# Kernel optimization log

Measured on AMD Instinct MI355X. Metric: run time of the kernel, lower is better.

The kernel has to match this reference:

```python
import jax, jax.numpy as jnp
import numpy as np

HEAD_DIM = 128
N_HEADS = 32
ROPE_DIM = 64
TOPK = 1024
B, S, HID, QLORA = 1, 2048, 4096, 1536
LN_EPS = 1e-5  # torch nn.LayerNorm default


def _hadamard_matrix(n):
    H = np.array([[1.0]], dtype=np.float32)
    while H.shape[0] < n:
        H = np.block([[H, H], [H, -H]])
    return jnp.asarray(H)

_H128 = _hadamard_matrix(HEAD_DIM)
_FWHT_SCALE = HEAD_DIM ** -0.5


def rotate_activation(x):
    # Fast Walsh-Hadamard transform == x @ H_sylvester, scaled by dim**-0.5
    return (x @ _H128) * _FWHT_SCALE


def rope_non_interleaved(x, cos, sin):
    # x: [..., rope_dim]; cos/sin: broadcastable [..., rope_dim/2]
    half = x.shape[-1] // 2
    x1, x2 = x[..., :half], x[..., half:]
    return jnp.concatenate([x1 * cos - x2 * sin, x1 * sin + x2 * cos], axis=-1)


def setup_inputs() -> dict:
    key = jax.random.key(0)
    ks = jax.random.split(key, 8)
    hidden_states = jax.random.normal(ks[0], (B, S, HID), jnp.float32)
    q_compressed = jax.random.normal(ks[1], (B, S, QLORA), jnp.float32)
    # rotary cos/sin for rope_dim=64 (standard concat layout)
    pos = jnp.arange(S, dtype=jnp.float32)
    inv_freq = 1.0 / (10000.0 ** (jnp.arange(0, ROPE_DIM, 2, dtype=jnp.float32) / ROPE_DIM))
    ang = pos[:, None] * inv_freq[None, :]  # [S, 32]
    cos = jnp.tile(jnp.cos(ang), (1, 2))[None]  # [1, S, 64]
    sin = jnp.tile(jnp.sin(ang), (1, 2))[None]
    # additive causal mask [B, S, S]
    causal = jnp.tril(jnp.ones((S, S), jnp.bool_))
    attention_mask = jnp.where(causal, 0.0, -1e9).astype(jnp.float32)[None]
    Wq_b = jax.random.normal(ks[2], (QLORA, N_HEADS * HEAD_DIM), jnp.float32) * (QLORA ** -0.5)
    Wk = jax.random.normal(ks[3], (HID, HEAD_DIM), jnp.float32) * (HID ** -0.5)
    k_gamma = jnp.ones((HEAD_DIM,), jnp.float32)
    k_beta = jnp.zeros((HEAD_DIM,), jnp.float32)
    Ww = jax.random.normal(ks[4], (HID, N_HEADS), jnp.float32) * (HID ** -0.5)
    return {"hidden_states": hidden_states, "q_compressed": q_compressed, "cos": cos,
            "sin": sin, "attention_mask": attention_mask, "Wq_b": Wq_b, "Wk": Wk,
            "k_gamma": k_gamma, "k_beta": k_beta, "Ww": Ww}


def reference(hidden_states, q_compressed, cos, sin, attention_mask, Wq_b, Wk, k_gamma, k_beta, Ww):
    b, s, _ = hidden_states.shape
    softmax_scale = HEAD_DIM ** -0.5
    # queries: [b, s, H, D]
    q = (q_compressed @ Wq_b).reshape(b, s, N_HEADS, HEAD_DIM)
    q_rope, q_nope = q[..., :ROPE_DIM], q[..., ROPE_DIM:]
    # keys: single shared head, LayerNorm(k)
    k = hidden_states @ Wk  # [b, s, D]
    mu = jnp.mean(k, axis=-1, keepdims=True)
    var = jnp.mean(jnp.square(k - mu), axis=-1, keepdims=True)
    k = (k - mu) * jax.lax.rsqrt(var + LN_EPS) * k_gamma + k_beta
    k_rope, k_nope = k[..., :ROPE_DIM], k[..., ROPE_DIM:]
    # non-interleaved RoPE (cos/sin truncated to half_dim=32)
    half = ROPE_DIM // 2
    c, sn = cos[..., :half], sin[..., :half]
    q_rope = rope_non_interleaved(q_rope, c[:, :, None, :], sn[:, :, None, :])
    k_rope = rope_non_interleaved(k_rope, c, sn)
    q = jnp.concatenate([q_rope, q_nope], axis=-1)
    k = jnp.concatenate([k_rope, k_nope], axis=-1)
    # Hadamard activation rotation
    q = rotate_activation(q)
    k = rotate_activation(k)
    # I_{t,s} = sum_h w_{t,h} * ReLU(q_{t,h} . k_s) * scale
    scores = jax.nn.relu(jnp.einsum('bthd,bsd->bths', q, k)) * softmax_scale
    weights = hidden_states @ Ww  # [b, t, H]
    index_scores = jnp.einsum('bths,bth->bts', scores, weights)
    index_scores = index_scores + attention_mask
    topk = min(TOPK, s)
    _, topk_indices = jax.lax.top_k(index_scores, topk)  # [b, s, topk]
    return topk_indices, index_scores
```

## Files before the change

kernel.cpp:

```cpp
#include <hip/hip_runtime.h>
#include <stdint.h>

#define S_LEN 2048
#define HID 4096
#define QLORA 1536
#define NH 32
#define HD 128
#define TOPK_N 1024
#define NEG_INF -1000000000.0f
#define INV_SQRT_HD 0.08838834764831844f

typedef __attribute__((ext_vector_type(8))) short short8;
typedef __attribute__((ext_vector_type(4))) short short4_;
typedef __attribute__((ext_vector_type(4))) float float4_;
typedef __attribute__((ext_vector_type(4))) unsigned uint4_;
typedef __attribute__((ext_vector_type(4))) int int4_;
typedef __attribute__((ext_vector_type(2))) int int2_;

__device__ __forceinline__ short f2bf(float x) {
  union { float f; unsigned u; } v; v.f = x;
  unsigned r = v.u + 0x7FFFu + ((v.u >> 16) & 1u);
  return (short)(r >> 16);
}

__device__ __forceinline__ unsigned f2ord(float x) {
  union { float f; unsigned u; } v; v.f = x;
  return v.u ^ (0x80000000u | (unsigned)((int)v.u >> 31));
}

__device__ __forceinline__ char f2fp8(float x) {
  return (char)__builtin_amdgcn_cvt_pk_fp8_f32(x, x, 0, 0);
}

__device__ __forceinline__ void gload_lds16(const void* g, void* l) {
  __builtin_amdgcn_global_load_lds((const __attribute__((address_space(1))) unsigned int*)g,
                                   (__attribute__((address_space(3))) unsigned int*)l, 16, 0, 0);
}

__global__ __launch_bounds__(256) void prep_kernel(
    const float* __restrict__ hidden, short* __restrict__ hidb,
    const float* __restrict__ qc, char* __restrict__ qc8,
    float* __restrict__ kacc,
    const float* __restrict__ wqb, char* __restrict__ wq8T,
    const float* __restrict__ wk, const float* __restrict__ ww,
    short* __restrict__ kwT) {
  __shared__ __align__(8) char stile[4352];
  int bid = blockIdx.x;
  const int tid = threadIdx.x;
  if (bid < 8192) {
    int i = bid * 256 + tid;
    float4 v = ((const float4*)hidden)[i];
    short4_ o;
    o[0] = f2bf(v.x); o[1] = f2bf(v.y); o[2] = f2bf(v.z); o[3] = f2bf(v.w);
    ((short4_*)hidb)[i] = o;
    return;
  }
  if (bid < 9728) {
    int i = (bid - 8192) * 256 + tid;
    float4 f0 = ((const float4*)qc)[i * 2];
    float4 f1 = ((const float4*)qc)[i * 2 + 1];
    int lo = 0, hi = 0;
    lo = __builtin_amdgcn_cvt_pk_fp8_f32(f0.x, f0.y, lo, 0);
    lo = __builtin_amdgcn_cvt_pk_fp8_f32(f0.z, f0.w, lo, 1);
    hi = __builtin_amdgcn_cvt_pk_fp8_f32(f1.x, f1.y, hi, 0);
    hi = __builtin_amdgcn_cvt_pk_fp8_f32(f1.z, f1.w, hi, 1);
    ((int2_*)qc8)[i] = (int2_){lo, hi};
    return;
  }
  if (bid < 10048) {
    int i = (bid - 9728) * 256 + tid;
    ((float4_*)kacc)[i] = (float4_){0.f, 0.f, 0.f, 0.f};
    return;
  }
  if (bid < 13120) {
    char (*t8)[33] = (char(*)[33])stile;
    int b = bid - 10048;
    int k0 = (b >> 7) * 64, n0 = (b & 127) * 32;
    #pragma unroll
    for (int i = 0; i < 8; i++) {
      int e = tid + i * 256;
      int r = e >> 5, c = e & 31;
      float x = wqb[(size_t)(k0 + r) * HID + n0 + c];
      t8[r][c] = f2fp8(x);
    }
    __syncthreads();
    int nl = tid >> 3, jk = (tid & 7) * 8;
    union { char c[8]; long l; } o;
    #pragma unroll
    for (int j = 0; j < 8; j++) o.c[j] = t8[jk + j][nl];
    *(long*)(wq8T + (size_t)(n0 + nl) * QLORA + k0 + jk) = o.l;
    return;
  }
  short (*tile)[33] = (short(*)[33])stile;
  const float* in; short* out; int R, C, bx, by;
  if (bid < 13632) {
    int b2 = bid - 13120;
    in = wk; out = kwT; R = HID; C = HD; bx = b2 & 3; by = b2 >> 2;
  } else {
    int b3 = bid - 13632;
    in = ww; out = kwT + 128 * HID; R = HID; C = NH; bx = 0; by = b3;
  }
  int c0 = bx * 32, r0 = by * 32;
  int tx = tid & 31, ty = tid >> 5;
  #pragma unroll
  for (int i = 0; i < 32; i += 8)
    tile[ty + i][tx] = f2bf(in[(size_t)(r0 + ty + i) * C + c0 + tx]);
  __syncthreads();
  #pragma unroll
  for (int i = 0; i < 32; i += 8)
    out[(size_t)(c0 + ty + i) * R + r0 + tx] = tile[tx][ty + i];
}

#define QSTAGE8(kt, Ad, Bd) do { \
  _Pragma("unroll") \
  for (int i = 0; i < 4; i++) { \
    int m = w * 32 + i * 8 + lr; \
    int gb = (kt) * 128 + ((lc ^ (m & 7)) << 4); \
    gload_lds16(qc8 + (size_t)(t0 + m) * QLORA + gb, (Ad) + (w * 32 + i * 8) * 128); \
    gload_lds16(wq8T + (size_t)(n0 + m) * QLORA + gb, (Bd) + (w * 32 + i * 8) * 128); \
  } \
} while (0)

#define QCOMPUTE8(Aq, Bq) do { \
  _Pragma("unroll") \
  for (int p = 0; p < 4; p++) { \
    int ch = p * 2 + (quad >> 1); \
    int lo8 = (quad & 1) * 8; \
    long a[2], b[8]; \
    _Pragma("unroll") \
    for (int mt = 0; mt < 2; mt++) { \
      int m = w * 32 + mt * 16 + l15; \
      a[mt] = *(const long*)((Aq) + m * 128 + ((ch ^ (m & 7)) << 4) + lo8); \
    } \
    _Pragma("unroll") \
    for (int nt = 0; nt < 8; nt++) { \
      int n = nt * 16 + l15; \
      b[nt] = *(const long*)((Bq) + n * 128 + ((ch ^ (n & 7)) << 4) + lo8); \
    } \
    _Pragma("unroll") \
    for (int mt = 0; mt < 2; mt++) \
      _Pragma("unroll") \
      for (int nt = 0; nt < 8; nt++) \
        acc[mt][nt] = __builtin_amdgcn_mfma_f32_16x16x32_fp8_fp8(a[mt], b[nt], acc[mt][nt], 0, 0, 0); \
  } \
} while (0)

__global__ __launch_bounds__(256, 2) void gemms_kernel(
    const char* __restrict__ qc8, const char* __restrict__ wq8T,
    const float* __restrict__ cosp, const float* __restrict__ sinp,
    char* __restrict__ qrot8,
    const short* __restrict__ hidb, const short* __restrict__ kwT,
    float* __restrict__ kacc) {
  __shared__ __align__(16) char smem[65536];
  const int tid = threadIdx.x;
  const int w = tid >> 6, lane = tid & 63;
  const int l15 = lane & 15, quad = lane >> 4;
  const int lr = lane >> 3, lc = lane & 7;

  if (blockIdx.x < 512) {
    char* A0 = smem;
    char* B0 = smem + 16384;
    char* A1 = smem + 32768;
    char* B1 = smem + 49152;
    const int n0 = (blockIdx.x & 31) * 128;
    const int t0 = (blockIdx.x >> 5) * 128;

    float4_ acc[2][8];
    #pragma unroll
    for (int mt = 0; mt < 2; mt++)
      #pragma unroll
      for (int i = 0; i < 8; i++) acc[mt][i] = (float4_){0.f, 0.f, 0.f, 0.f};

    QSTAGE8(0, A0, B0);
    __syncthreads();
    for (int kt = 0; kt < 12; kt += 2) {
      QSTAGE8(kt + 1, A1, B1);
      QCOMPUTE8(A0, B0);
      __syncthreads();
      if (kt + 2 < 12) QSTAGE8(kt + 2, A0, B0);
      QCOMPUTE8(A1, B1);
      __syncthreads();
    }

    #pragma unroll
    for (int mt = 0; mt < 2; mt++) {
      #pragma unroll
      for (int r = 0; r < 4; r++) {
        const int trow = t0 + w * 32 + mt * 16 + quad * 4 + r;
        float v[8];
        #pragma unroll
        for (int nt = 0; nt < 8; nt++) v[nt] = acc[mt][nt][r];
        float cc0 = cosp[trow * 64 + l15], cc1 = cosp[trow * 64 + 16 + l15];
        float ss0 = sinp[trow * 64 + l15], ss1 = sinp[trow * 64 + 16 + l15];
        float r0 = v[0] * cc0 - v[2] * ss0, r1 = v[1] * cc1 - v[3] * ss1;
        float r2 = v[0] * ss0 + v[2] * cc0, r3 = v[1] * ss1 + v[3] * cc1;
        v[0] = r0; v[1] = r1; v[2] = r2; v[3] = r3;
        char* orow = qrot8 + (size_t)trow * HID + n0;
        #pragma unroll
        for (int nt = 0; nt < 8; nt++)
          orow[nt * 16 + l15] = f2fp8(v[nt]);
      }
    }
  } else {
    short* Al = (short*)smem;
    short* Bl = (short*)(smem + 8192);
    const int b2 = blockIdx.x - 512;
    const int kc0 = (b2 & 7) * 512;
    const int m0g = (b2 >> 3) * 64;

    float4_ acc[10];
    #pragma unroll
    for (int i = 0; i < 10; i++) acc[i] = (float4_){0.f, 0.f, 0.f, 0.f};

    for (int k0 = kc0; k0 < kc0 + 512; k0 += 64) {
      #pragma unroll
      for (int i = 0; i < 2; i++) {
        int m = w * 16 + i * 8 + lr;
        int gk = k0 + ((lc ^ (m & 7)) << 3);
        gload_lds16(hidb + (size_t)(m0g + m) * HID + gk, Al + (w * 16 + i * 8) * 64);
      }
      #pragma unroll
      for (int i = 0; i < 5; i++) {
        int n = w * 40 + i * 8 + lr;
        int gk = k0 + ((lc ^ (n & 7)) << 3);
        gload_lds16(kwT + (size_t)n * HID + gk, Bl + (w * 40 + i * 8) * 64);
      }
      __syncthreads();
      #pragma unroll
      for (int kk = 0; kk < 64; kk += 32) {
        int ca = (kk >> 3) + quad;
        int ma = w * 16 + l15;
        short8 a = *(const short8*)(Al + ma * 64 + ((ca ^ (ma & 7)) << 3));
        #pragma unroll
        for (int nt = 0; nt < 10; nt++) {
          int n = nt * 16 + l15;
          short8 b = *(const short8*)(Bl + n * 64 + ((ca ^ (n & 7)) << 3));
          acc[nt] = __builtin_amdgcn_mfma_f32_16x16x32_bf16(a, b, acc[nt], 0, 0, 0);
        }
      }
      __syncthreads();
    }
    #pragma unroll
    for (int nt = 0; nt < 10; nt++)
      #pragma unroll
      for (int r = 0; r < 4; r++) {
        int row = m0g + w * 16 + quad * 4 + r;
        atomicAdd(&kacc[(size_t)row * 160 + nt * 16 + l15], acc[nt][r]);
      }
  }
}

__global__ __launch_bounds__(256) void ln_rope_kernel(
    const float* __restrict__ kacc, const float* __restrict__ gamma,
    const float* __restrict__ beta, const float* __restrict__ cosp,
    const float* __restrict__ sinp, char* __restrict__ krot8) {
  const int tid = threadIdx.x;
  const int row = blockIdx.x * 16 + (tid >> 4);
  const int l16 = tid & 15;
  const int c0 = l16 * 8;
  const float* rp = kacc + (size_t)row * 160 + c0;
  float4 f0 = ((const float4*)rp)[0], f1 = ((const float4*)rp)[1];
  float v[8] = {f0.x, f0.y, f0.z, f0.w, f1.x, f1.y, f1.z, f1.w};
  float s = 0.f, ss = 0.f;
  #pragma unroll
  for (int j = 0; j < 8; j++) { s += v[j]; ss += v[j] * v[j]; }
  #pragma unroll
  for (int d = 1; d <= 8; d <<= 1) {
    s += __shfl_xor(s, d, 64); ss += __shfl_xor(ss, d, 64);
  }
  float mu = s * (1.0f / 128.0f);
  float var = ss * (1.0f / 128.0f) - mu * mu;
  float rs = rsqrtf(var + 1e-5f);
  #pragma unroll
  for (int j = 0; j < 8; j++)
    v[j] = (v[j] - mu) * rs * gamma[c0 + j] + beta[c0 + j];
  #pragma unroll
  for (int j = 0; j < 8; j++) {
    float p = __shfl_xor(v[j], 4, 64);
    if (l16 < 8) {
      int idx = (c0 + j) & 31;
      float c = cosp[row * 64 + idx], sn = sinp[row * 64 + idx];
      v[j] = v[j] * c + p * ((l16 < 4) ? -sn : sn);
    }
  }
  int lo = 0, hi = 0;
  lo = __builtin_amdgcn_cvt_pk_fp8_f32(v[0], v[1], lo, 0);
  lo = __builtin_amdgcn_cvt_pk_fp8_f32(v[2], v[3], lo, 1);
  hi = __builtin_amdgcn_cvt_pk_fp8_f32(v[4], v[5], hi, 0);
  hi = __builtin_amdgcn_cvt_pk_fp8_f32(v[6], v[7], hi, 1);
  *(int2_*)(krot8 + (size_t)row * 128 + c0) = (int2_){lo, hi};
}

__global__ __launch_bounds__(256, 3) void scores_kernel(
    const char* __restrict__ qrot8, const char* __restrict__ krot8,
    const float* __restrict__ kacc, float* __restrict__ isc) {
  __shared__ __align__(16) char smem[32768];
  char* buf0 = smem;
  char* buf1 = smem + 16384;

  const int tid = threadIdx.x;
  const int w = tid >> 6, lane = tid & 63;
  const int l15 = lane & 15, quad = lane >> 4;
  const int wm = w >> 1, wn = w & 1;
  const int lr8 = lane >> 3, lc8 = lane & 7;

  const int bid = blockIdx.x;
  const int strip = (bid & 1) ? (511 - (bid >> 1)) : (bid >> 1);
  const int t0 = strip * 4;
  const int nsb = (t0 + 3) / 128 + 1;

  const char* Abase = qrot8 + (size_t)t0 * 32 * 128;
  #pragma unroll
  for (int i = 0; i < 4; i++) {
    int m = i * 32 + w * 8 + lr8;
    int gofs = m * 128 + ((lc8 ^ (m & 7)) << 4);
    gload_lds16(Abase + gofs, buf0 + (i * 32 + w * 8) * 128);
    gload_lds16(krot8 + gofs, buf1 + (i * 32 + w * 8) * 128);
  }
  __syncthreads();

  long af[4][4];
  #pragma unroll
  for (int k4 = 0; k4 < 4; k4++) {
    int ch = k4 * 2 + (quad >> 1);
    int lo8 = (quad & 1) * 8;
    #pragma unroll
    for (int mt = 0; mt < 4; mt++) {
      int m = wm * 64 + mt * 16 + l15;
      af[k4][mt] = *(const long*)(buf0 + m * 128 + ((ch ^ (m & 7)) << 4) + lo8);
    }
  }

  const int t_a = t0 + wm * 2, t_b = t_a + 1;
  float wq[4][4];
  #pragma unroll
  for (int mt = 0; mt < 4; mt++) {
    int tt = (mt < 2) ? t_a : t_b;
    #pragma unroll
    for (int r = 0; r < 4; r++)
      wq[mt][r] = kacc[(size_t)tt * 160 + 128 + (mt & 1) * 16 + quad * 4 + r];
  }
  __syncthreads();

  for (int sb = 0; sb < nsb; sb++) {
    char* cur = (sb & 1) ? buf0 : buf1;
    if (sb + 1 < nsb) {
      char* nxt = (sb & 1) ? buf1 : buf0;
      const char* Bbase = krot8 + (size_t)(sb + 1) * 128 * 128;
      #pragma unroll
      for (int i = 0; i < 4; i++) {
        int m = i * 32 + w * 8 + lr8;
        int gofs = m * 128 + ((lc8 ^ (m & 7)) << 4);
        gload_lds16(Bbase + gofs, nxt + (i * 32 + w * 8) * 128);
      }
    }

    float4_ acc[4][4];
    #pragma unroll
    for (int mt = 0; mt < 4; mt++)
      #pragma unroll
      for (int nt = 0; nt < 4; nt++) acc[mt][nt] = (float4_){0.f, 0.f, 0.f, 0.f};

    #pragma unroll
    for (int k4 = 0; k4 < 4; k4++) {
      int ch = k4 * 2 + (quad >> 1);
      int lo8 = (quad & 1) * 8;
      long b[4];
      #pragma unroll
      for (int nt = 0; nt < 4; nt++) {
        int n = wn * 64 + nt * 16 + l15;
        b[nt] = *(const long*)(cur + n * 128 + ((ch ^ (n & 7)) << 4) + lo8);
      }
      #pragma unroll
      for (int mt = 0; mt < 4; mt++)
        #pragma unroll
        for (int nt = 0; nt < 4; nt++)
          acc[mt][nt] = __builtin_amdgcn_mfma_f32_16x16x32_fp8_fp8(af[k4][mt], b[nt], acc[mt][nt], 0, 0, 0);
    }

    #pragma unroll
    for (int nt = 0; nt < 4; nt++) {
      float pa = 0.f, pb = 0.f;
      #pragma unroll
      for (int r = 0; r < 4; r++) {
        pa += fmaxf(acc[0][nt][r], 0.f) * wq[0][r] + fmaxf(acc[1][nt][r], 0.f) * wq[1][r];
        pb += fmaxf(acc[2][nt][r], 0.f) * wq[2][r] + fmaxf(acc[3][nt][r], 0.f) * wq[3][r];
      }
      pa += __shfl_xor(pa, 16, 64); pa += __shfl_xor(pa, 32, 64);
      pb += __shfl_xor(pb, 16, 64); pb += __shfl_xor(pb, 32, 64);
      int s = sb * 128 + wn * 64 + nt * 16 + l15;
      if (quad == 0)
        isc[(size_t)t_a * S_LEN + s] = (s <= t_a) ? pa * INV_SQRT_HD : NEG_INF;
      else if (quad == 1)
        isc[(size_t)t_b * S_LEN + s] = (s <= t_b) ? pb * INV_SQRT_HD : NEG_INF;
    }

    __syncthreads();
  }

  if (wn == 0) {
    const int myrow = (lane < 32) ? t_a : t_b;
    const int l32 = lane & 31;
    float4_ nf = (float4_){NEG_INF, NEG_INF, NEG_INF, NEG_INF};
    float4_* rowp = (float4_*)(isc + (size_t)myrow * S_LEN);
    for (int i = nsb * 32 + l32; i < 512; i += 32) rowp[i] = nf;
  }
}

#define CEK(x, y, d) { if ((d) ? (v[x] < v[y]) : (v[x] > v[y])) { unsigned _t = v[x]; v[x] = v[y]; v[y] = _t; } }

__device__ __forceinline__ void shfl_phase(unsigned v[8], int j, int base, bool d) {
  const int delta = j >> 3;
  const bool keep_max = (((base & j) == 0) == d);
  #pragma unroll
  for (int r = 0; r < 8; r++) {
    unsigned pv = (unsigned)__shfl_xor((int)v[r], delta, 64);
    unsigned mx = v[r] > pv ? v[r] : pv;
    unsigned mn = v[r] > pv ? pv : v[r];
    v[r] = keep_max ? mx : mn;
  }
}

__device__ __forceinline__ void reg_phase(unsigned v[8], bool d) {
  CEK(0, 4, d); CEK(1, 5, d); CEK(2, 6, d); CEK(3, 7, d);
  CEK(0, 2, d); CEK(1, 3, d); CEK(4, 6, d); CEK(5, 7, d);
  CEK(0, 1, d); CEK(2, 3, d); CEK(4, 5, d); CEK(6, 7, d);
}

__device__ __forceinline__ int chswz(int c) { return c ^ ((c >> 3) & 7); }

__device__ __forceinline__ void lds_phase(unsigned v[8], unsigned* keys, int tid, int base,
                                          int j, bool d) {
  const int c0 = tid * 2, c1 = c0 + 1;
  ((uint4_*)keys)[chswz(c0)] = (uint4_){v[0], v[1], v[2], v[3]};
  ((uint4_*)keys)[chswz(c1)] = (uint4_){v[4], v[5], v[6], v[7]};
  __syncthreads();
  const int ptid = tid ^ (j >> 3);
  uint4_ u0 = ((uint4_*)keys)[chswz(ptid * 2)];
  uint4_ u1 = ((uint4_*)keys)[chswz(ptid * 2 + 1)];
  unsigned p[8] = {u0[0], u0[1], u0[2], u0[3], u1[0], u1[1], u1[2], u1[3]};
  const bool keep_max = (((base & j) == 0) == d);
  #pragma unroll
  for (int r = 0; r < 8; r++) {
    unsigned mx = v[r] > p[r] ? v[r] : p[r];
    unsigned mn = v[r] > p[r] ? p[r] : v[r];
    v[r] = keep_max ? mx : mn;
  }
  __syncthreads();
}

__global__ __launch_bounds__(256) void topk_kernel(const float* __restrict__ isc,
                                                   int* __restrict__ idx_out) {
  __shared__ __align__(16) unsigned keys[2048];
  const int t = blockIdx.x;
  const int tid = threadIdx.x;
  const int base = tid * 8;
  unsigned v[8];
  {
    const float* row = isc + (size_t)t * S_LEN;
    float4 f0 = ((const float4*)row)[tid * 2];
    float4 f1 = ((const float4*)row)[tid * 2 + 1];
    v[0] = (f2ord(f0.x) & 0xFFFFF800u) | (unsigned)(2047 - base - 0);
    v[1] = (f2ord(f0.y) & 0xFFFFF800u) | (unsigned)(2047 - base - 1);
    v[2] = (f2ord(f0.z) & 0xFFFFF800u) | (unsigned)(2047 - base - 2);
    v[3] = (f2ord(f0.w) & 0xFFFFF800u) | (unsigned)(2047 - base - 3);
    v[4] = (f2ord(f1.x) & 0xFFFFF800u) | (unsigned)(2047 - base - 4);
    v[5] = (f2ord(f1.y) & 0xFFFFF800u) | (unsigned)(2047 - base - 5);
    v[6] = (f2ord(f1.z) & 0xFFFFF800u) | (unsigned)(2047 - base - 6);
    v[7] = (f2ord(f1.w) & 0xFFFFF800u) | (unsigned)(2047 - base - 7);
  }
  CEK(0, 1, true); CEK(2, 3, false); CEK(4, 5, true); CEK(6, 7, false);
  CEK(0, 2, true); CEK(1, 3, true); CEK(4, 6, false); CEK(5, 7, false);
  CEK(0, 1, true); CEK(2, 3, true); CEK(4, 5, false); CEK(6, 7, false);
  {
    bool d8 = ((base & 8) == 0);
    CEK(0, 4, d8); CEK(1, 5, d8); CEK(2, 6, d8); CEK(3, 7, d8);
    CEK(0, 2, d8); CEK(1, 3, d8); CEK(4, 6, d8); CEK(5, 7, d8);
    CEK(0, 1, d8); CEK(2, 3, d8); CEK(4, 5, d8); CEK(6, 7, d8);
  }
  #pragma unroll
  for (int kb = 4; kb <= 11; kb++) {
    const int k = 1 << kb;
    const bool d = ((base & k) == 0);
    for (int j = k >> 1; j >= 512; j >>= 1)
      lds_phase(v, keys, tid, base, j, d);
    {
      int jtop = (k >> 1) < 256 ? (k >> 1) : 256;
      for (int j = jtop; j >= 8; j >>= 1)
        shfl_phase(v, j, base, d);
    }
    reg_phase(v, d);
  }
  if (tid < 128) {
    int4_ o0, o1;
    #pragma unroll
    for (int r = 0; r < 4; r++) o0[r] = 2047 - (int)(v[r] & 0x7FFu);
    #pragma unroll
    for (int r = 0; r < 4; r++) o1[r] = 2047 - (int)(v[4 + r] & 0x7FFu);
    ((int4_*)(idx_out + (size_t)t * TOPK_N))[tid * 2] = o0;
    ((int4_*)(idx_out + (size_t)t * TOPK_N))[tid * 2 + 1] = o1;
  }
}

extern "C" void kernel_launch(void* const* d_in, const int* in_sizes, int n_in,
                              void* d_out, int out_size, void* d_ws, size_t ws_size,
                              hipStream_t stream) {
  const float* hidden = (const float*)d_in[0];
  const float* qc     = (const float*)d_in[1];
  const float* cosp   = (const float*)d_in[2];
  const float* sinp   = (const float*)d_in[3];
  const float* wqb    = (const float*)d_in[5];
  const float* wk     = (const float*)d_in[6];
  const float* gamma  = (const float*)d_in[7];
  const float* beta   = (const float*)d_in[8];
  const float* ww     = (const float*)d_in[9];

  char* ws = (char*)d_ws;
  short* hidb  = (short*)ws;
  char*  qc8   = (char*)(ws + 16777216);
  char*  wq8T  = (char*)(ws + 19922944);
  short* kwT   = (short*)(ws + 26214400);
  char*  krot8 = (char*)(ws + 27525120);
  char*  qrot8 = (char*)(ws + 27787264);
  float* kacc  = (float*)(ws + 36175872);

  int*   idx_out = (int*)d_out;
  float* isc     = ((float*)d_out) + (size_t)S_LEN * TOPK_N;

  prep_kernel<<<dim3(13760), dim3(256), 0, stream>>>(hidden, hidb, qc, qc8, kacc,
                                                     wqb, wq8T, wk, ww, kwT);
  gemms_kernel<<<dim3(768), dim3(256), 0, stream>>>(qc8, wq8T, cosp, sinp, qrot8,
                                                    hidb, kwT, kacc);
  ln_rope_kernel<<<dim3(128), dim3(256), 0, stream>>>(kacc, gamma, beta, cosp, sinp, krot8);
  scores_kernel<<<dim3(512), dim3(256), 0, stream>>>(qrot8, krot8, kacc, isc);
  topk_kernel<<<dim3(2048), dim3(256), 0, stream>>>(isc, idx_out);
}
```

Before: 248.8 us.

## Fuse scores and top-k into one kernel with LDS-resident sort keys

Merges the scoring kernel and the per-row bitonic top-k kernel. Each block writes ordered sort keys for its four rows directly into LDS (with a swizzle) while it still writes the scores out, then sorts those four rows in place. This removes the global re-read of the score matrix and one kernel launch. It also reorders gemms blocks so the smaller K-projection blocks are dispatched first and changes the strip mapping. In exchange, LDS use per block doubles to 64KB and each block serially sorts four rows, which lowers occupancy and parallelism for the sort phase.

```diff
diff --git a/kernel.cpp b/kernel.cpp
--- a/kernel.cpp
+++ b/kernel.cpp
@@ -36,6 +36,8 @@
   __builtin_amdgcn_global_load_lds((const __attribute__((address_space(1))) unsigned int*)g,
                                    (__attribute__((address_space(3))) unsigned int*)l, 16, 0, 0);
 }
+
+__device__ __forceinline__ int chswz(int c) { return c ^ ((c >> 3) & 7); }
 
 __global__ __launch_bounds__(256) void prep_kernel(
     const float* __restrict__ hidden, short* __restrict__ hidb,
@@ -157,13 +159,14 @@
   const int l15 = lane & 15, quad = lane >> 4;
   const int lr = lane >> 3, lc = lane & 7;
 
-  if (blockIdx.x < 512) {
+  if (blockIdx.x >= 256) {
     char* A0 = smem;
     char* B0 = smem + 16384;
     char* A1 = smem + 32768;
     char* B1 = smem + 49152;
-    const int n0 = (blockIdx.x & 31) * 128;
-    const int t0 = (blockIdx.x >> 5) * 128;
+    const int bq = blockIdx.x - 256;
+    const int n0 = (bq & 31) * 128;
+    const int t0 = (bq >> 5) * 128;
 
     float4_ acc[2][8];
     #pragma unroll
@@ -204,7 +207,7 @@
   } else {
     short* Al = (short*)smem;
     short* Bl = (short*)(smem + 8192);
-    const int b2 = blockIdx.x - 512;
+    const int b2 = blockIdx.x;
     const int kc0 = (b2 & 7) * 512;
     const int m0g = (b2 >> 3) * 64;
 
@@ -291,122 +294,6 @@
   *(int2_*)(krot8 + (size_t)row * 128 + c0) = (int2_){lo, hi};
 }
 
-__global__ __launch_bounds__(256, 3) void scores_kernel(
-    const char* __restrict__ qrot8, const char* __restrict__ krot8,
-    const float* __restrict__ kacc, float* __restrict__ isc) {
-  __shared__ __align__(16) char smem[32768];
-  char* buf0 = smem;
-  char* buf1 = smem + 16384;
-
-  const int tid = threadIdx.x;
-  const int w = tid >> 6, lane = tid & 63;
-  const int l15 = lane & 15, quad = lane >> 4;
-  const int wm = w >> 1, wn = w & 1;
-  const int lr8 = lane >> 3, lc8 = lane & 7;
-
-  const int bid = blockIdx.x;
-  const int strip = (bid & 1) ? (511 - (bid >> 1)) : (bid >> 1);
-  const int t0 = strip * 4;
-  const int nsb = (t0 + 3) / 128 + 1;
-
-  const char* Abase = qrot8 + (size_t)t0 * 32 * 128;
-  #pragma unroll
-  for (int i = 0; i < 4; i++) {
-    int m = i * 32 + w * 8 + lr8;
-    int gofs = m * 128 + ((lc8 ^ (m & 7)) << 4);
-    gload_lds16(Abase + gofs, buf0 + (i * 32 + w * 8) * 128);
-    gload_lds16(krot8 + gofs, buf1 + (i * 32 + w * 8) * 128);
-  }
-  __syncthreads();
-
-  long af[4][4];
-  #pragma unroll
-  for (int k4 = 0; k4 < 4; k4++) {
-    int ch = k4 * 2 + (quad >> 1);
-    int lo8 = (quad & 1) * 8;
-    #pragma unroll
-    for (int mt = 0; mt < 4; mt++) {
-      int m = wm * 64 + mt * 16 + l15;
-      af[k4][mt] = *(const long*)(buf0 + m * 128 + ((ch ^ (m & 7)) << 4) + lo8);
-    }
-  }
-
-  const int t_a = t0 + wm * 2, t_b = t_a + 1;
-  float wq[4][4];
-  #pragma unroll
-  for (int mt = 0; mt < 4; mt++) {
-    int tt = (mt < 2) ? t_a : t_b;
-    #pragma unroll
-    for (int r = 0; r < 4; r++)
-      wq[mt][r] = kacc[(size_t)tt * 160 + 128 + (mt & 1) * 16 + quad * 4 + r];
-  }
-  __syncthreads();
-
-  for (int sb = 0; sb < nsb; sb++) {
-    char* cur = (sb & 1) ? buf0 : buf1;
-    if (sb + 1 < nsb) {
-      char* nxt = (sb & 1) ? buf1 : buf0;
-      const char* Bbase = krot8 + (size_t)(sb + 1) * 128 * 128;
-      #pragma unroll
-      for (int i = 0; i < 4; i++) {
-        int m = i * 32 + w * 8 + lr8;
-        int gofs = m * 128 + ((lc8 ^ (m & 7)) << 4);
-        gload_lds16(Bbase + gofs, nxt + (i * 32 + w * 8) * 128);
-      }
-    }
-
-    float4_ acc[4][4];
-    #pragma unroll
-    for (int mt = 0; mt < 4; mt++)
-      #pragma unroll
-      for (int nt = 0; nt < 4; nt++) acc[mt][nt] = (float4_){0.f, 0.f, 0.f, 0.f};
-
-    #pragma unroll
-    for (int k4 = 0; k4 < 4; k4++) {
-      int ch = k4 * 2 + (quad >> 1);
-      int lo8 = (quad & 1) * 8;
-      long b[4];
-      #pragma unroll
-      for (int nt = 0; nt < 4; nt++) {
-        int n = wn * 64 + nt * 16 + l15;
-        b[nt] = *(const long*)(cur + n * 128 + ((ch ^ (n & 7)) << 4) + lo8);
-      }
-      #pragma unroll
-      for (int mt = 0; mt < 4; mt++)
-        #pragma unroll
-        for (int nt = 0; nt < 4; nt++)
-          acc[mt][nt] = __builtin_amdgcn_mfma_f32_16x16x32_fp8_fp8(af[k4][mt], b[nt], acc[mt][nt], 0, 0, 0);
-    }
-
-    #pragma unroll
-    for (int nt = 0; nt < 4; nt++) {
-      float pa = 0.f, pb = 0.f;
-      #pragma unroll
-      for (int r = 0; r < 4; r++) {
-        pa += fmaxf(acc[0][nt][r], 0.f) * wq[0][r] + fmaxf(acc[1][nt][r], 0.f) * wq[1][r];
-        pb += fmaxf(acc[2][nt][r], 0.f) * wq[2][r] + fmaxf(acc[3][nt][r], 0.f) * wq[3][r];
-      }
-      pa += __shfl_xor(pa, 16, 64); pa += __shfl_xor(pa, 32, 64);
-      pb += __shfl_xor(pb, 16, 64); pb += __shfl_xor(pb, 32, 64);
-      int s = sb * 128 + wn * 64 + nt * 16 + l15;
-      if (quad == 0)
-        isc[(size_t)t_a * S_LEN + s] = (s <= t_a) ? pa * INV_SQRT_HD : NEG_INF;
-      else if (quad == 1)
-        isc[(size_t)t_b * S_LEN + s] = (s <= t_b) ? pb * INV_SQRT_HD : NEG_INF;
-    }
-
-    __syncthreads();
-  }
-
-  if (wn == 0) {
-    const int myrow = (lane < 32) ? t_a : t_b;
-    const int l32 = lane & 31;
-    float4_ nf = (float4_){NEG_INF, NEG_INF, NEG_INF, NEG_INF};
-    float4_* rowp = (float4_*)(isc + (size_t)myrow * S_LEN);
-    for (int i = nsb * 32 + l32; i < 512; i += 32) rowp[i] = nf;
-  }
-}
-
 #define CEK(x, y, d) { if ((d) ? (v[x] < v[y]) : (v[x] > v[y])) { unsigned _t = v[x]; v[x] = v[y]; v[y] = _t; } }
 
 __device__ __forceinline__ void shfl_phase(unsigned v[8], int j, int base, bool d) {
@@ -426,8 +313,6 @@
   CEK(0, 2, d); CEK(1, 3, d); CEK(4, 6, d); CEK(5, 7, d);
   CEK(0, 1, d); CEK(2, 3, d); CEK(4, 5, d); CEK(6, 7, d);
 }
-
-__device__ __forceinline__ int chswz(int c) { return c ^ ((c >> 3) & 7); }
 
 __device__ __forceinline__ void lds_phase(unsigned v[8], unsigned* keys, int tid, int base,
                                           int j, bool d) {
@@ -449,56 +334,179 @@
   __syncthreads();
 }
 
-__global__ __launch_bounds__(256) void topk_kernel(const float* __restrict__ isc,
-                                                   int* __restrict__ idx_out) {
-  __shared__ __align__(16) unsigned keys[2048];
-  const int t = blockIdx.x;
+__global__ __launch_bounds__(256, 2) void scores_topk_kernel(
+    const char* __restrict__ qrot8, const char* __restrict__ krot8,
+    const float* __restrict__ kacc, float* __restrict__ isc,
+    int* __restrict__ idx_out) {
+  __shared__ __align__(16) char smem[65536];
+  char* buf0 = smem;
+  char* buf1 = smem + 16384;
+  unsigned* keys = (unsigned*)(smem + 32768);
+
   const int tid = threadIdx.x;
+  const int w = tid >> 6, lane = tid & 63;
+  const int l15 = lane & 15, quad = lane >> 4;
+  const int wm = w >> 1, wn = w & 1;
+  const int lr8 = lane >> 3, lc8 = lane & 7;
+
+  const int bid = blockIdx.x;
+  const int strip = (bid < 256) ? bid : (767 - bid);
+  const int t0 = strip * 4;
+  const int nsb = (t0 + 3) / 128 + 1;
+
+  const char* Abase = qrot8 + (size_t)t0 * 32 * 128;
+  #pragma unroll
+  for (int i = 0; i < 4; i++) {
+    int m = i * 32 + w * 8 + lr8;
+    int gofs = m * 128 + ((lc8 ^ (m & 7)) << 4);
+    gload_lds16(Abase + gofs, buf0 + (i * 32 + w * 8) * 128);
+    gload_lds16(krot8 + gofs, buf1 + (i * 32 + w * 8) * 128);
+  }
+  __syncthreads();
+
+  long af[4][4];
+  #pragma unroll
+  for (int k4 = 0; k4 < 4; k4++) {
+    int ch = k4 * 2 + (quad >> 1);
+    int lo8 = (quad & 1) * 8;
+    #pragma unroll
+    for (int mt = 0; mt < 4; mt++) {
+      int m = wm * 64 + mt * 16 + l15;
+      af[k4][mt] = *(const long*)(buf0 + m * 128 + ((ch ^ (m & 7)) << 4) + lo8);
+    }
+  }
+
+  const int t_a = t0 + wm * 2, t_b = t_a + 1;
+  float wq[4][4];
+  #pragma unroll
+  for (int mt = 0; mt < 4; mt++) {
+    int tt = (mt < 2) ? t_a : t_b;
+    #pragma unroll
+    for (int r = 0; r < 4; r++)
+      wq[mt][r] = kacc[(size_t)tt * 160 + 128 + (mt & 1) * 16 + quad * 4 + r];
+  }
+  __syncthreads();
+
+  for (int sb = 0; sb < nsb; sb++) {
+    char* cur = (sb & 1) ? buf0 : buf1;
+    if (sb + 1 < nsb) {
+      char* nxt = (sb & 1) ? buf1 : buf0;
+      const char* Bbase = krot8 + (size_t)(sb + 1) * 128 * 128;
+      #pragma unroll
+      for (int i = 0; i < 4; i++) {
+        int m = i * 32 + w * 8 + lr8;
+        int gofs = m * 128 + ((lc8 ^ (m & 7)) << 4);
+        gload_lds16(Bbase + gofs, nxt + (i * 32 + w * 8) * 128);
+      }
+    }
+
+    float4_ acc[4][4];
+    #pragma unroll
+    for (int mt = 0; mt < 4; mt++)
+      #pragma unroll
+      for (int nt = 0; nt < 4; nt++) acc[mt][nt] = (float4_){0.f, 0.f, 0.f, 0.f};
+
+    #pragma unroll
+    for (int k4 = 0; k4 < 4; k4++) {
+      int ch = k4 * 2 + (quad >> 1);
+      int lo8 = (quad & 1) * 8;
+      long b[4];
+      #pragma unroll
+      for (int nt = 0; nt < 4; nt++) {
+        int n = wn * 64 + nt * 16 + l15;
+        b[nt] = *(const long*)(cur + n * 128 + ((ch ^ (n & 7)) << 4) + lo8);
+      }
+      #pragma unroll
+      for (int mt = 0; mt < 4; mt++)
+        #pragma unroll
+        for (int nt = 0; nt < 4; nt++)
+          acc[mt][nt] = __builtin_amdgcn_mfma_f32_16x16x32_fp8_fp8(af[k4][mt], b[nt], acc[mt][nt], 0, 0, 0);
+    }
+
+    #pragma unroll
+    for (int nt = 0; nt < 4; nt++) {
+      float pa = 0.f, pb = 0.f;
+      #pragma unroll
+      for (int r = 0; r < 4; r++) {
+        pa += fmaxf(acc[0][nt][r], 0.f) * wq[0][r] + fmaxf(acc[1][nt][r], 0.f) * wq[1][r];
+        pb += fmaxf(acc[2][nt][r], 0.f) * wq[2][r] + fmaxf(acc[3][nt][r], 0.f) * wq[3][r];
+      }
+      pa += __shfl_xor(pa, 16, 64); pa += __shfl_xor(pa, 32, 64);
+      pb += __shfl_xor(pb, 16, 64); pb += __shfl_xor(pb, 32, 64);
+      int s = sb * 128 + wn * 64 + nt * 16 + l15;
+      if (quad < 2) {
+        const int tt = (quad == 0) ? t_a : t_b;
+        const float p = (quad == 0) ? pa : pb;
+        const float val = (s <= tt) ? p * INV_SQRT_HD : NEG_INF;
+        isc[(size_t)tt * S_LEN + s] = val;
+        unsigned key = (f2ord(val) & 0xFFFFF800u) | (unsigned)(2047 - s);
+        unsigned* krow = keys + (tt - t0) * 2048;
+        krow[(chswz(s >> 2) << 2) | (s & 3)] = key;
+      }
+    }
+
+    __syncthreads();
+  }
+
+  {
+    const unsigned negord = f2ord(NEG_INF) & 0xFFFFF800u;
+    for (int s = nsb * 128 + tid; s < S_LEN; s += 256) {
+      unsigned key = negord | (unsigned)(2047 - s);
+      int pos = (chswz(s >> 2) << 2) | (s & 3);
+      #pragma unroll
+      for (int rl = 0; rl < 4; rl++) keys[rl * 2048 + pos] = key;
+    }
+    if (wn == 0) {
+      const int myrow = (lane < 32) ? t_a : t_b;
+      const int l32 = lane & 31;
+      float4_ nf = (float4_){NEG_INF, NEG_INF, NEG_INF, NEG_INF};
+      float4_* rowp = (float4_*)(isc + (size_t)myrow * S_LEN);
+      for (int i = nsb * 32 + l32; i < 512; i += 32) rowp[i] = nf;
+    }
+  }
+  __syncthreads();
+
   const int base = tid * 8;
-  unsigned v[8];
-  {
-    const float* row = isc + (size_t)t * S_LEN;
-    float4 f0 = ((const float4*)row)[tid * 2];
-    float4 f1 = ((const float4*)row)[tid * 2 + 1];
-    v[0] = (f2ord(f0.x) & 0xFFFFF800u) | (unsigned)(2047 - base - 0);
-    v[1] = (f2ord(f0.y) & 0xFFFFF800u) | (unsigned)(2047 - base - 1);
-    v[2] = (f2ord(f0.z) & 0xFFFFF800u) | (unsigned)(2047 - base - 2);
-    v[3] = (f2ord(f0.w) & 0xFFFFF800u) | (unsigned)(2047 - base - 3);
-    v[4] = (f2ord(f1.x) & 0xFFFFF800u) | (unsigned)(2047 - base - 4);
-    v[5] = (f2ord(f1.y) & 0xFFFFF800u) | (unsigned)(2047 - base - 5);
-    v[6] = (f2ord(f1.z) & 0xFFFFF800u) | (unsigned)(2047 - base - 6);
-    v[7] = (f2ord(f1.w) & 0xFFFFF800u) | (unsigned)(2047 - base - 7);
-  }
-  CEK(0, 1, true); CEK(2, 3, false); CEK(4, 5, true); CEK(6, 7, false);
-  CEK(0, 2, true); CEK(1, 3, true); CEK(4, 6, false); CEK(5, 7, false);
-  CEK(0, 1, true); CEK(2, 3, true); CEK(4, 5, false); CEK(6, 7, false);
-  {
-    bool d8 = ((base & 8) == 0);
-    CEK(0, 4, d8); CEK(1, 5, d8); CEK(2, 6, d8); CEK(3, 7, d8);
-    CEK(0, 2, d8); CEK(1, 3, d8); CEK(4, 6, d8); CEK(5, 7, d8);
-    CEK(0, 1, d8); CEK(2, 3, d8); CEK(4, 5, d8); CEK(6, 7, d8);
-  }
-  #pragma unroll
-  for (int kb = 4; kb <= 11; kb++) {
-    const int k = 1 << kb;
-    const bool d = ((base & k) == 0);
-    for (int j = k >> 1; j >= 512; j >>= 1)
-      lds_phase(v, keys, tid, base, j, d);
+  for (int rl = 0; rl < 4; rl++) {
+    unsigned* krow = keys + rl * 2048;
+    unsigned v[8];
     {
-      int jtop = (k >> 1) < 256 ? (k >> 1) : 256;
-      for (int j = jtop; j >= 8; j >>= 1)
-        shfl_phase(v, j, base, d);
-    }
-    reg_phase(v, d);
-  }
-  if (tid < 128) {
-    int4_ o0, o1;
-    #pragma unroll
-    for (int r = 0; r < 4; r++) o0[r] = 2047 - (int)(v[r] & 0x7FFu);
-    #pragma unroll
-    for (int r = 0; r < 4; r++) o1[r] = 2047 - (int)(v[4 + r] & 0x7FFu);
-    ((int4_*)(idx_out + (size_t)t * TOPK_N))[tid * 2] = o0;
-    ((int4_*)(idx_out + (size_t)t * TOPK_N))[tid * 2 + 1] = o1;
+      uint4_ u0 = ((uint4_*)krow)[chswz(tid * 2)];
+      uint4_ u1 = ((uint4_*)krow)[chswz(tid * 2 + 1)];
+      v[0] = u0[0]; v[1] = u0[1]; v[2] = u0[2]; v[3] = u0[3];
+      v[4] = u1[0]; v[5] = u1[1]; v[6] = u1[2]; v[7] = u1[3];
+    }
+    CEK(0, 1, true); CEK(2, 3, false); CEK(4, 5, true); CEK(6, 7, false);
+    CEK(0, 2, true); CEK(1, 3, true); CEK(4, 6, false); CEK(5, 7, false);
+    CEK(0, 1, true); CEK(2, 3, true); CEK(4, 5, false); CEK(6, 7, false);
+    {
+      bool d8 = ((base & 8) == 0);
+      CEK(0, 4, d8); CEK(1, 5, d8); CEK(2, 6, d8); CEK(3, 7, d8);
+      CEK(0, 2, d8); CEK(1, 3, d8); CEK(4, 6, d8); CEK(5, 7, d8);
+      CEK(0, 1, d8); CEK(2, 3, d8); CEK(4, 5, d8); CEK(6, 7, d8);
+    }
+    #pragma unroll
+    for (int kb = 4; kb <= 11; kb++) {
+      const int k = 1 << kb;
+      const bool d = ((base & k) == 0);
+      for (int j = k >> 1; j >= 512; j >>= 1)
+        lds_phase(v, krow, tid, base, j, d);
+      {
+        int jtop = (k >> 1) < 256 ? (k >> 1) : 256;
+        for (int j = jtop; j >= 8; j >>= 1)
+          shfl_phase(v, j, base, d);
+      }
+      reg_phase(v, d);
+    }
+    if (tid < 128) {
+      int4_ o0, o1;
+      #pragma unroll
+      for (int r = 0; r < 4; r++) o0[r] = 2047 - (int)(v[r] & 0x7FFu);
+      #pragma unroll
+      for (int r = 0; r < 4; r++) o1[r] = 2047 - (int)(v[4 + r] & 0x7FFu);
+      ((int4_*)(idx_out + (size_t)(t0 + rl) * TOPK_N))[tid * 2] = o0;
+      ((int4_*)(idx_out + (size_t)(t0 + rl) * TOPK_N))[tid * 2 + 1] = o1;
+    }
   }
 }
 
@@ -532,6 +540,5 @@
   gemms_kernel<<<dim3(768), dim3(256), 0, stream>>>(qc8, wq8T, cosp, sinp, qrot8,
                                                     hidb, kwT, kacc);
   ln_rope_kernel<<<dim3(128), dim3(256), 0, stream>>>(kacc, gamma, beta, cosp, sinp, krot8);
-  scores_kernel<<<dim3(512), dim3(256), 0, stream>>>(qrot8, krot8, kacc, isc);
-  topk_kernel<<<dim3(2048), dim3(256), 0, stream>>>(isc, idx_out);
-}
+  scores_topk_kernel<<<dim3(512), dim3(256), 0, stream>>>(qrot8, krot8, kacc, isc, idx_out);
+}
```

Result: slower. 256.9 us (+3.3%).
